# Performance work log

Hardware: AMD Instinct MI355X
Metric: run time of the kernel (lower is better)

## Reference

```python
import jax, jax.numpy as jnp
import numpy as np

MAX_SEQ_LEN = 65536
DISCOUNT_FACTOR = 0.99
ADVANTAGE_LAMBDA = 0.95


def _init_lambda_sequence(target_mean, seq_len):
    # mirrors LearnableTD._create_init_lambda_sequence
    initial = 2.0 * target_mean - 1.0
    final = 1.0
    if initial < 0:
        initial = 0.0
        final = 2.0 * target_mean
    lam = np.zeros(seq_len, dtype=np.float32)
    lam[:-1] = np.linspace(initial, final, seq_len - 1, dtype=np.float32)
    lam[-1] = 1.0
    # clip so atanh stays finite (torch atanh(1.0) -> inf)
    return np.clip(lam, 0.0, 1.0 - 1e-6)


def setup_inputs() -> dict:
    lam = _init_lambda_sequence(ADVANTAGE_LAMBDA, MAX_SEQ_LEN)
    raw_gamma = jnp.arctanh(jnp.full((1,), DISCOUNT_FACTOR, dtype=jnp.float32))
    raw_lambd = jnp.arctanh(jnp.asarray(lam, dtype=jnp.float32))
    return {"raw_gamma": raw_gamma, "raw_lambd": raw_lambd}


def reference(raw_gamma, raw_lambd):
    # LearnableTD.update_sum_reward_weights
    gamma = jnp.maximum(jnp.tanh(raw_gamma), 0.0)[0]      # scalar
    lambd = jnp.maximum(jnp.tanh(raw_lambd), 0.0)          # [S]

    # backward affine recurrence: v_t = gamma*(1 - l_t + l_t * v_{t+1}), v_S = 1
    def step(v_next, l_t):
        v_t = gamma * (1.0 - l_t + l_t * v_next)
        w_t = jnp.maximum(1.0 - v_t, 1e-8)
        return v_t, w_t

    _, raw_w = jax.lax.scan(step, jnp.float32(1.0), lambd, reverse=True)
    raw_w = raw_w[None, :, None]                            # [1, S, 1]
    scale = 1.0 / jnp.maximum(jnp.mean(raw_w), 1e-8)
    return scale * raw_w
```

## Files before the change

kernel.cpp:

```cpp
#include <hip/hip_runtime.h>

#define N_ELEMS 65536
#define NBLK    256
#define BTH     256
#define CHK     0x5F3759DFu


__device__ __forceinline__ float fast_tanh_pos(float x) {
    const float t = __expf(2.0f * x);
    return (t - 1.0f) * __builtin_amdgcn_rcpf(t + 1.0f);
}

__device__ __forceinline__ void wave_suffix_scan(float& A, float& B, int lane) {
#pragma unroll
    for (int d = 1; d < 64; d <<= 1) {
        const float A2 = __shfl_down(A, d, 64);
        const float B2 = __shfl_down(B, d, 64);
        if (lane + d < 64) { B = fmaf(A, B2, B); A = A * A2; }
    }
}

__device__ __forceinline__ void pub_store(unsigned* p, unsigned v) {
    __hip_atomic_store(p, v, __ATOMIC_RELAXED, __HIP_MEMORY_SCOPE_AGENT);
}
__device__ __forceinline__ unsigned pub_load(const unsigned* p) {
    return __hip_atomic_load(p, __ATOMIC_RELAXED, __HIP_MEMORY_SCOPE_AGENT);
}

__global__ __launch_bounds__(BTH) void fused_td_kernel(
        const float* __restrict__ raw_gamma,
        const float* __restrict__ raw_lambd,
        float* __restrict__ out,
        unsigned* __restrict__ pub) {
    const int tid  = threadIdx.x;
    const int lane = tid & 63;
    const int w    = tid >> 6;
    const int bid  = blockIdx.x;

    __shared__ float sA[4], sB[4], sSA[4], sSB[4], sTerm[4];
    __shared__ float sVI[NBLK];

    const float gamma = fmaxf(fast_tanh_pos(raw_gamma[0]), 0.0f);

    const int g = bid * BTH + tid;
    const float lam = fmaxf(fast_tanh_pos(raw_lambd[g]), 0.0f);
    const float a   = gamma * lam;

    float A = a, B = gamma - a;
    wave_suffix_scan(A, B, lane);
    if (lane == 0) { sA[w] = A; sB[w] = B; }
    __syncthreads();
    float TA = 1.0f, TB = 0.0f;
    for (int j = w + 1; j < 4; ++j) { TB = fmaf(TA, sB[j], TB); TA *= sA[j]; }
    const float fA = A * TA;
    const float fB = fmaf(A, TB, B);

    float rA = fA, rB = fB;
#pragma unroll
    for (int off = 32; off > 0; off >>= 1) {
        rA += __shfl_down(rA, off, 64);
        rB += __shfl_down(rB, off, 64);
    }
    if (lane == 0) { sSA[w] = rA; sSB[w] = rB; }
    __syncthreads();

    if (tid == 0) {
        const float bSA = (sSA[0] + sSA[1]) + (sSA[2] + sSA[3]);
        const float bSB = (sSB[0] + sSB[1]) + (sSB[2] + sSB[3]);
        const unsigned v0 = __float_as_uint(fA);
        const unsigned v1 = __float_as_uint(fB);
        const unsigned v2 = __float_as_uint(bSA);
        const unsigned v3 = __float_as_uint(bSB);
        pub_store(&pub[0 * NBLK + bid], v0);
        pub_store(&pub[1 * NBLK + bid], v1);
        pub_store(&pub[2 * NBLK + bid], v2);
        pub_store(&pub[3 * NBLK + bid], v3);
        pub_store(&pub[4 * NBLK + bid], v0 ^ CHK);
        pub_store(&pub[5 * NBLK + bid], v1 ^ CHK);
        pub_store(&pub[6 * NBLK + bid], v2 ^ CHK);
        pub_store(&pub[7 * NBLK + bid], v3 ^ CHK);
    }

    unsigned u0, u1, u2, u3;
    for (;;) {
        u0 = pub_load(&pub[0 * NBLK + tid]);
        u1 = pub_load(&pub[1 * NBLK + tid]);
        u2 = pub_load(&pub[2 * NBLK + tid]);
        u3 = pub_load(&pub[3 * NBLK + tid]);
        const unsigned c0 = pub_load(&pub[4 * NBLK + tid]);
        const unsigned c1 = pub_load(&pub[5 * NBLK + tid]);
        const unsigned c2 = pub_load(&pub[6 * NBLK + tid]);
        const unsigned c3 = pub_load(&pub[7 * NBLK + tid]);
        if (((u0 ^ c0) == CHK) && ((u1 ^ c1) == CHK) &&
            ((u2 ^ c2) == CHK) && ((u3 ^ c3) == CHK))
            break;
        __builtin_amdgcn_s_sleep(1);
    }
    float bA  = __uint_as_float(u0);
    float bB  = __uint_as_float(u1);
    const float bSA = __uint_as_float(u2);
    const float bSB = __uint_as_float(u3);

    __syncthreads();

    wave_suffix_scan(bA, bB, lane);
    if (lane == 0) { sA[w] = bA; sB[w] = bB; }
    __syncthreads();
    float CA = bA, CB = bB;
    for (int j = w + 1; j < 4; ++j) { CB = fmaf(CA, sB[j], CB); CA *= sA[j]; }
    sVI[tid] = CA + CB;
    __syncthreads();

    const float vin_t = (tid == NBLK - 1) ? 1.0f : sVI[tid + 1];
    float term = fmaf(bSA, vin_t, bSB);
#pragma unroll
    for (int off = 32; off > 0; off >>= 1)
        term += __shfl_xor(term, off, 64);
    if (lane == 0) sTerm[w] = term;
    __syncthreads();
    const float sum_v  = (sTerm[0] + sTerm[1]) + (sTerm[2] + sTerm[3]);
    const float mean_w = ((float)N_ELEMS - sum_v) * (1.0f / (float)N_ELEMS);
    const float scale  = 1.0f / fmaxf(mean_w, 1e-8f);

    const float v_blk = (bid == NBLK - 1) ? 1.0f : sVI[bid + 1];
    const float v  = fmaf(fA, v_blk, fB);
    const float wq = fmaxf(1.0f - v, 1e-8f);
    out[g] = scale * wq;
}

extern "C" void kernel_launch(void* const* d_in, const int* in_sizes, int n_in,
                              void* d_out, int out_size, void* d_ws, size_t ws_size,
                              hipStream_t stream) {
    const float* raw_gamma = (const float*)d_in[0];
    const float* raw_lambd = (const float*)d_in[1];
    float* out = (float*)d_out;
    unsigned* pub = (unsigned*)d_ws;

    fused_td_kernel<<<NBLK, BTH, 0, stream>>>(raw_gamma, raw_lambd, out, pub);
}
```

Measured before the change: 10.85 us.

## Use 64 blocks of 1024 threads with packed 64-bit checked flags

Reshapes the grid from 256 blocks of 256 threads to 64 blocks of 1024 threads. The cross-block carry exchange then fits in a single wavefront, and only wave 0 polls, scans and reduces the block summaries. Each value and its check word are packed into one 64-bit atomic store, which halves the number of published and polled words and removes two block barriers. In exchange, each block runs a longer 16-wave intra-block combine, and occupancy per CU changes.

```diff
diff --git a/kernel.cpp b/kernel.cpp
--- a/kernel.cpp
+++ b/kernel.cpp
@@ -1,8 +1,9 @@
 #include <hip/hip_runtime.h>
 
 #define N_ELEMS 65536
-#define NBLK    256
-#define BTH     256
+#define NBLK    64
+#define BTH     1024
+#define NWAVE   (BTH / 64)
 #define CHK     0x5F3759DFu
 
 
@@ -20,10 +21,17 @@
     }
 }
 
-__device__ __forceinline__ void pub_store(unsigned* p, unsigned v) {
+__device__ __forceinline__ unsigned long long pack_chk(float f) {
+    const unsigned u = __float_as_uint(f);
+    return (unsigned long long)u | ((unsigned long long)(u ^ CHK) << 32);
+}
+
+__device__ __forceinline__ void pub_store(unsigned long long* p,
+                                          unsigned long long v) {
     __hip_atomic_store(p, v, __ATOMIC_RELAXED, __HIP_MEMORY_SCOPE_AGENT);
 }
-__device__ __forceinline__ unsigned pub_load(const unsigned* p) {
+__device__ __forceinline__ unsigned long long pub_load(
+        const unsigned long long* p) {
     return __hip_atomic_load(p, __ATOMIC_RELAXED, __HIP_MEMORY_SCOPE_AGENT);
 }
 
@@ -31,14 +39,14 @@
         const float* __restrict__ raw_gamma,
         const float* __restrict__ raw_lambd,
         float* __restrict__ out,
-        unsigned* __restrict__ pub) {
+        unsigned long long* __restrict__ pub) {
     const int tid  = threadIdx.x;
     const int lane = tid & 63;
     const int w    = tid >> 6;
     const int bid  = blockIdx.x;
 
-    __shared__ float sA[4], sB[4], sSA[4], sSB[4], sTerm[4];
-    __shared__ float sVI[NBLK];
+    __shared__ float sA[NWAVE], sB[NWAVE], sSA[NWAVE], sSB[NWAVE];
+    __shared__ float sVblk, sScale;
 
     const float gamma = fmaxf(fast_tanh_pos(raw_gamma[0]), 0.0f);
 
@@ -50,8 +58,15 @@
     wave_suffix_scan(A, B, lane);
     if (lane == 0) { sA[w] = A; sB[w] = B; }
     __syncthreads();
+
+    float tA[NWAVE], tB[NWAVE];
+#pragma unroll
+    for (int j = 0; j < NWAVE; ++j) { tA[j] = sA[j]; tB[j] = sB[j]; }
     float TA = 1.0f, TB = 0.0f;
-    for (int j = w + 1; j < 4; ++j) { TB = fmaf(TA, sB[j], TB); TA *= sA[j]; }
+#pragma unroll
+    for (int j = 0; j < NWAVE; ++j) {
+        if (j > w) { TB = fmaf(TA, tB[j], TB); TA *= tA[j]; }
+    }
     const float fA = A * TA;
     const float fB = fmaf(A, TB, B);
 
@@ -65,67 +80,57 @@
     __syncthreads();
 
     if (tid == 0) {
-        const float bSA = (sSA[0] + sSA[1]) + (sSA[2] + sSA[3]);
-        const float bSB = (sSB[0] + sSB[1]) + (sSB[2] + sSB[3]);
-        const unsigned v0 = __float_as_uint(fA);
-        const unsigned v1 = __float_as_uint(fB);
-        const unsigned v2 = __float_as_uint(bSA);
-        const unsigned v3 = __float_as_uint(bSB);
-        pub_store(&pub[0 * NBLK + bid], v0);
-        pub_store(&pub[1 * NBLK + bid], v1);
-        pub_store(&pub[2 * NBLK + bid], v2);
-        pub_store(&pub[3 * NBLK + bid], v3);
-        pub_store(&pub[4 * NBLK + bid], v0 ^ CHK);
-        pub_store(&pub[5 * NBLK + bid], v1 ^ CHK);
-        pub_store(&pub[6 * NBLK + bid], v2 ^ CHK);
-        pub_store(&pub[7 * NBLK + bid], v3 ^ CHK);
+        float bSA = 0.0f, bSB = 0.0f;
+#pragma unroll
+        for (int j = 0; j < NWAVE; ++j) { bSA += sSA[j]; bSB += sSB[j]; }
+        pub_store(&pub[0 * NBLK + bid], pack_chk(fA));
+        pub_store(&pub[1 * NBLK + bid], pack_chk(fB));
+        pub_store(&pub[2 * NBLK + bid], pack_chk(bSA));
+        pub_store(&pub[3 * NBLK + bid], pack_chk(bSB));
     }
 
-    unsigned u0, u1, u2, u3;
-    for (;;) {
-        u0 = pub_load(&pub[0 * NBLK + tid]);
-        u1 = pub_load(&pub[1 * NBLK + tid]);
-        u2 = pub_load(&pub[2 * NBLK + tid]);
-        u3 = pub_load(&pub[3 * NBLK + tid]);
-        const unsigned c0 = pub_load(&pub[4 * NBLK + tid]);
-        const unsigned c1 = pub_load(&pub[5 * NBLK + tid]);
-        const unsigned c2 = pub_load(&pub[6 * NBLK + tid]);
-        const unsigned c3 = pub_load(&pub[7 * NBLK + tid]);
-        if (((u0 ^ c0) == CHK) && ((u1 ^ c1) == CHK) &&
-            ((u2 ^ c2) == CHK) && ((u3 ^ c3) == CHK))
-            break;
-        __builtin_amdgcn_s_sleep(1);
+    if (w == 0) {
+        float bA, bB, cSA, cSB;
+        for (;;) {
+            const unsigned long long q0 = pub_load(&pub[0 * NBLK + lane]);
+            const unsigned long long q1 = pub_load(&pub[1 * NBLK + lane]);
+            const unsigned long long q2 = pub_load(&pub[2 * NBLK + lane]);
+            const unsigned long long q3 = pub_load(&pub[3 * NBLK + lane]);
+            const bool ok =
+                ((unsigned)(q0 >> 32) == ((unsigned)q0 ^ CHK)) &&
+                ((unsigned)(q1 >> 32) == ((unsigned)q1 ^ CHK)) &&
+                ((unsigned)(q2 >> 32) == ((unsigned)q2 ^ CHK)) &&
+                ((unsigned)(q3 >> 32) == ((unsigned)q3 ^ CHK));
+            if (ok) {
+                bA  = __uint_as_float((unsigned)q0);
+                bB  = __uint_as_float((unsigned)q1);
+                cSA = __uint_as_float((unsigned)q2);
+                cSB = __uint_as_float((unsigned)q3);
+                break;
+            }
+            __builtin_amdgcn_s_sleep(2);
+        }
+
+        wave_suffix_scan(bA, bB, lane);
+        const float S   = bA + bB;
+        float vin = __shfl_down(S, 1, 64);
+        if (lane == 63) vin = 1.0f;
+
+        float term = fmaf(cSA, vin, cSB);
+#pragma unroll
+        for (int off = 32; off > 0; off >>= 1)
+            term += __shfl_xor(term, off, 64);
+        const float mean_w = ((float)N_ELEMS - term) * (1.0f / (float)N_ELEMS);
+        const float scale  = 1.0f / fmaxf(mean_w, 1e-8f);
+        const float v_blk  = __shfl(vin, bid, 64);
+
+        if (lane == 0) { sVblk = v_blk; sScale = scale; }
     }
-    float bA  = __uint_as_float(u0);
-    float bB  = __uint_as_float(u1);
-    const float bSA = __uint_as_float(u2);
-    const float bSB = __uint_as_float(u3);
-
     __syncthreads();
 
-    wave_suffix_scan(bA, bB, lane);
-    if (lane == 0) { sA[w] = bA; sB[w] = bB; }
-    __syncthreads();
-    float CA = bA, CB = bB;
-    for (int j = w + 1; j < 4; ++j) { CB = fmaf(CA, sB[j], CB); CA *= sA[j]; }
-    sVI[tid] = CA + CB;
-    __syncthreads();
-
-    const float vin_t = (tid == NBLK - 1) ? 1.0f : sVI[tid + 1];
-    float term = fmaf(bSA, vin_t, bSB);
-#pragma unroll
-    for (int off = 32; off > 0; off >>= 1)
-        term += __shfl_xor(term, off, 64);
-    if (lane == 0) sTerm[w] = term;
-    __syncthreads();
-    const float sum_v  = (sTerm[0] + sTerm[1]) + (sTerm[2] + sTerm[3]);
-    const float mean_w = ((float)N_ELEMS - sum_v) * (1.0f / (float)N_ELEMS);
-    const float scale  = 1.0f / fmaxf(mean_w, 1e-8f);
-
-    const float v_blk = (bid == NBLK - 1) ? 1.0f : sVI[bid + 1];
-    const float v  = fmaf(fA, v_blk, fB);
+    const float v  = fmaf(fA, sVblk, fB);
     const float wq = fmaxf(1.0f - v, 1e-8f);
-    out[g] = scale * wq;
+    out[g] = sScale * wq;
 }
 
 extern "C" void kernel_launch(void* const* d_in, const int* in_sizes, int n_in,
@@ -134,7 +139,7 @@
     const float* raw_gamma = (const float*)d_in[0];
     const float* raw_lambd = (const float*)d_in[1];
     float* out = (float*)d_out;
-    unsigned* pub = (unsigned*)d_ws;
+    unsigned long long* pub = (unsigned long long*)d_ws;
 
     fused_td_kernel<<<NBLK, BTH, 0, stream>>>(raw_gamma, raw_lambd, out, pub);
 }
```

Result: faster. 10.53 us (-3.0%).
